# Performance work log

Hardware: AMD Instinct MI355X
Metric: run time of the kernel (lower is better)

The kernel has to match this reference:

```python
import jax, jax.numpy as jnp
import numpy as np

FS = 100
KERNEL = FS * 3 + 1  # 301, matches nn.AvgPool1d(kernel_size, stride=1, padding=K//2, count_include_pad=True)


def _avg_pool1d(x, k):
    # x: [B, L] -> same-length moving average with zero padding counted in the divisor
    w = jnp.full((1, 1, k), 1.0 / k, dtype=x.dtype)
    y = jax.lax.conv_general_dilated(
        x[:, None, :], w, window_strides=(1,), padding=[(k // 2, k // 2)],
        dimension_numbers=("NCH", "OIH", "NCH"))
    return y[:, 0, :]


def _unwrap_phase(phase):
    # torch-faithful np.unwrap: [B, L]
    d = jnp.diff(phase, axis=-1)
    dm = jnp.mod(d + jnp.pi, 2.0 * jnp.pi) - jnp.pi
    dm = jnp.where((dm == -jnp.pi) & (d > 0), jnp.pi, dm)
    offset = jnp.cumsum(d - dm, axis=-1)
    unwrapped = jnp.concatenate([phase[..., :1], phase[..., 1:] + offset], axis=-1)
    return jnp.nan_to_num(unwrapped, nan=0.0)


def _normalize(x):
    # zero mean, unit (unbiased, like torch.std) variance along last dim
    n = x.shape[-1]
    mean = jnp.mean(x, axis=-1, keepdims=True)
    var = jnp.sum((x - mean) ** 2, axis=-1, keepdims=True) / (n - 1)
    return (x - mean) / (jnp.sqrt(var) + 1e-5)


def setup_inputs() -> dict:
    key = jax.random.key(0)
    k1, k2 = jax.random.split(key)
    B, L = 64, 262144
    return {
        "radar_i": jax.random.normal(k1, (B, L), dtype=jnp.float32),
        "radar_q": jax.random.normal(k2, (B, L), dtype=jnp.float32),
    }


def reference(radar_i, radar_q):
    magnitude = jnp.nan_to_num(jnp.sqrt(radar_i ** 2 + radar_q ** 2), nan=0.0)
    phase = jnp.nan_to_num(jnp.arctan2(radar_q, radar_i), nan=0.0)
    phase_unwrap = _unwrap_phase(phase)
    phase_filt = phase_unwrap - _avg_pool1d(phase_unwrap, KERNEL)
    magnitude_filt = magnitude - _avg_pool1d(magnitude, KERNEL)
    magnitude_norm = jnp.nan_to_num(_normalize(magnitude_filt), nan=0.0)
    phase_norm = jnp.nan_to_num(_normalize(phase_filt), nan=0.0)
    return jnp.stack([magnitude_norm, phase_norm], axis=1)  # [B, 2, L]
```

## Files before the change

### kernel.cpp

```cpp
#include <hip/hip_runtime.h>
#include <math.h>
#include <stdint.h>

#define TPB 256
constexpr int Bn = 64;
constexpr int Ln = 262144;
constexpr int S  = 2048;
constexpr int NC = Ln / S;
constexpr int HA = S + 301;
constexpr int EPT = 11;
constexpr int OPT = S / TPB;
constexpr int NF4 = 641;
constexpr int LDSZ = 2820;
constexpr int NW = TPB / 64;

constexpr float TWO_PI_F = 6.28318530717958647692f;
constexpr float PI_F = 3.14159265358979323846f;
constexpr float HALF_PI_F = 1.57079632679489661923f;
constexpr float INV_TWO_PI_F = 0.15915494309189533577f;

__device__ __forceinline__ int wrap_k(float d) {
    float kf = floorf(__fmaf_rn(d, INV_TWO_PI_F, 0.5f));
    float dm = __fmaf_rn(-kf, TWO_PI_F, d);
    if (dm == -PI_F && d > 0.f) kf -= 1.f;
    return (int)kf;
}

__device__ __forceinline__ float fast_atan2f(float q, float i) {
    float aq = fabsf(q), ai = fabsf(i);
    float mx = fmaxf(aq, ai), mn = fminf(aq, ai);
    float r = __builtin_amdgcn_rcpf(mx);
    r = r * (2.0f - mx * r);
    float t = mn * r;
    if (mx == 0.f) t = 0.f;
    float s = t * t;
    float p = __fmaf_rn(s, 0.0028662257f, -0.0161657367f);
    p = __fmaf_rn(p, s,  0.0429096138f);
    p = __fmaf_rn(p, s, -0.0752896400f);
    p = __fmaf_rn(p, s,  0.1065626393f);
    p = __fmaf_rn(p, s, -0.1420889944f);
    p = __fmaf_rn(p, s,  0.1999355085f);
    p = __fmaf_rn(p, s, -0.3333314528f);
    float at = __fmaf_rn(p * s, t, t);
    if (aq > ai) at = HALF_PI_F - at;
    if (i < 0.f) at = PI_F - at;
    return (q < 0.f) ? -at : at;
}

__device__ __forceinline__ void gload_lds16(const float* g, float* lds_base) {
    __builtin_amdgcn_global_load_lds(
        (__attribute__((address_space(1))) void*)(uintptr_t)(const void*)g,
        (__attribute__((address_space(3))) void*)(uintptr_t)(void*)lds_base,
        16, 0, 0);
}

__global__ __launch_bounds__(TPB, 7) void k_filt(const float* __restrict__ Ig,
                                                 const float* __restrict__ Qg,
                                                 int* __restrict__ Ag,
                                                 int* __restrict__ Bg,
                                                 float* __restrict__ out,
                                                 float* __restrict__ PS) {
    __shared__ __align__(16) float sI_s[LDSZ];
    __shared__ __align__(16) float sQ_s[LDSZ];
    __shared__ int iwt[NW];
    __shared__ float fwt[NW];
    __shared__ float fwt2[NW];
    __shared__ float rbuf[NW][4];
    float* spu = sI_s + 1;
    float* smg = sQ_s + 1;

    const int c = blockIdx.x, b = blockIdx.y;
    const int t0 = c * S;
    const int base = t0 - 151;
    const int astart = base - 1;
    const int tid = threadIdx.x;
    const int lane = tid & 63, wid = tid >> 6;
    const bool edge = (c == 0) | (c == NC - 1);
    const float* Ib = Ig + (size_t)b * Ln;
    const float* Qb = Qg + (size_t)b * Ln;

    if (!edge) {
        const float* gI = Ib + astart;
        const float* gQ = Qb + astart;
#pragma unroll
        for (int k = wid; k < 11; k += NW) {
            int f = k * 64 + lane;
            if (f < NF4) {
                gload_lds16(gI + 4 * f, sI_s + k * 256);
                gload_lds16(gQ + 4 * f, sQ_s + k * 256);
            }
        }
    } else {
#pragma unroll
        for (int j = 0; j < 10; ++j) {
            int k = tid + j * TPB;
            int g = astart + k;
            float a = 0.f, q = 0.f;
            if (g >= 0 && g < Ln) { a = Ib[g]; q = Qb[g]; }
            sI_s[k] = a;
            sQ_s[k] = q;
        }
    }
    __syncthreads();

    const int seg = tid * EPT;
    const int kb = seg;
    const int gs = astart + kb;

    float ph[12], mg[12];
#pragma unroll
    for (int i = 0; i < 12; ++i) {
        float a = sI_s[kb + i], q = sQ_s[kb + i];
        ph[i] = fast_atan2f(q, a);
        mg[i] = __builtin_amdgcn_sqrtf(__fmaf_rn(a, a, q * q));
    }

    int kloc[12];
    kloc[0] = 0;
    float rm = 0.f;
    {
        int run = 0;
#pragma unroll
        for (int i = 1; i < 12; ++i) {
            run += wrap_k(ph[i] - ph[i - 1]);
            kloc[i] = run;
            rm += mg[i];
        }
    }

    int vi_ = kloc[11];
    float vf = rm;
#pragma unroll
    for (int o = 1; o < 64; o <<= 1) {
        int ui = __shfl_up(vi_, o, 64);
        float uf = __shfl_up(vf, o, 64);
        if (lane >= o) { vi_ += ui; vf += uf; }
    }
    if (lane == 63) { iwt[wid] = vi_; fwt[wid] = vf; }
    __syncthreads();
    int addi = 0; float addf = 0.f;
#pragma unroll
    for (int w = 0; w < NW; ++w) {
        addi += (w < wid) ? iwt[w] : 0;
        addf += (w < wid) ? fwt[w] : 0.f;
    }
    const int excl = vi_ - kloc[11] + addi;
    const float em = vf - rm + addf;

    if (tid == 13)  Ag[b * NC + c] = excl + kloc[8];
    if (tid == 199) Bg[b * NC + c] = excl + kloc[10];

    float rp = 0.f;
    if (!edge) {
#pragma unroll
        for (int i = 1; i < 12; ++i)
            rp += __fmaf_rn((float)(excl + kloc[i]), TWO_PI_F, ph[i]);
    } else {
#pragma unroll
        for (int i = 1; i < 12; ++i) {
            int g = gs + i;
            if (g >= 0 && g < Ln)
                rp += __fmaf_rn((float)(excl + kloc[i]), TWO_PI_F, ph[i]);
        }
    }

    float incf = rp;
#pragma unroll
    for (int o = 1; o < 64; o <<= 1) {
        float uf = __shfl_up(incf, o, 64);
        if (lane >= o) incf += uf;
    }
    if (lane == 63) fwt2[wid] = incf;
    __syncthreads();
    float addp = 0.f;
#pragma unroll
    for (int w = 0; w < NW; ++w) addp += (w < wid) ? fwt2[w] : 0.f;
    const float ep = incf - rp + addp;

    if (!edge) {
        float runp = ep, runm = em;
#pragma unroll
        for (int i = 1; i < 12; ++i) {
            int li = seg + i - 1;
            runp += __fmaf_rn((float)(excl + kloc[i]), TWO_PI_F, ph[i]);
            spu[li] = runp;
            runm += mg[i];
            smg[li] = runm;
        }
    } else {
        float runp = ep, runm = em;
#pragma unroll
        for (int i = 1; i < 12; ++i) {
            int li = seg + i - 1;
            int g = gs + i;
            float v = 0.f;
            if (g >= 0 && g < Ln)
                v = __fmaf_rn((float)(excl + kloc[i]), TWO_PI_F, ph[i]);
            runp += v;
            spu[li] = runp;
            runm += mg[i];
            smg[li] = runm;
        }
    }
    __syncthreads();

    float s1mf = 0.f, s2mf = 0.f, s1pf = 0.f, s2pf = 0.f;
    float* om = out + ((size_t)b * 2) * Ln + t0;
    float* op = out + ((size_t)b * 2 + 1) * Ln + t0;
    constexpr float INV_K = 1.0f / 301.0f;
#pragma unroll
    for (int j = 0; j < OPT; ++j) {
        int t = tid + j * TPB;
        int lt = t + 151;
        float Mq = smg[lt - 151], Mm = smg[lt - 1], Ml = smg[lt], Mp = smg[lt + 150];
        float Pq = spu[lt - 151], Pm = spu[lt - 1], Pl = spu[lt], Pp = spu[lt + 150];
        float fm = (Ml - Mm) - (Mp - Mq) * INV_K;
        float fp = (Pl - Pm) - (Pp - Pq) * INV_K;
        om[t] = fm;
        op[t] = fp;
        s1mf += fm; s2mf = __fmaf_rn(fm, fm, s2mf);
        s1pf += fp; s2pf = __fmaf_rn(fp, fp, s2pf);
    }
#pragma unroll
    for (int o = 32; o > 0; o >>= 1) {
        s1mf += __shfl_down(s1mf, o, 64);
        s2mf += __shfl_down(s2mf, o, 64);
        s1pf += __shfl_down(s1pf, o, 64);
        s2pf += __shfl_down(s2pf, o, 64);
    }
    if (lane == 0) { rbuf[wid][0] = s1mf; rbuf[wid][1] = s2mf; rbuf[wid][2] = s1pf; rbuf[wid][3] = s2pf; }
    __syncthreads();
    if (tid == 0) {
        float t0f = 0.f, t1f = 0.f, t2f = 0.f, t3f = 0.f;
#pragma unroll
        for (int w = 0; w < NW; ++w) {
            t0f += rbuf[w][0]; t1f += rbuf[w][1]; t2f += rbuf[w][2]; t3f += rbuf[w][3];
        }
        float* p = PS + (size_t)(b * NC + c) * 4;
        p[0] = t0f; p[1] = t1f; p[2] = t2f; p[3] = t3f;
    }
}

__global__ void k_post(const int* __restrict__ Ag, const int* __restrict__ Bg,
                       float* __restrict__ out, const float* __restrict__ PS,
                       float* __restrict__ ROW) {
    const int b = blockIdx.x;
    const int lane = threadIdx.x;
    const int idx = b * NC;

    int w = (Bg[idx + lane] - Ag[idx + lane]);
    if (lane + 64 < NC - 1) w += (Bg[idx + 64 + lane] - Ag[idx + 64 + lane]);
#pragma unroll
    for (int o = 32; o > 0; o >>= 1) w += __shfl_down(w, o, 64);
    int O = __shfl(w, 0, 64);
    int aL = Ag[idx + NC - 1];
    float C = TWO_PI_F * (float)(O - aL);

    constexpr float INV_K = 1.0f / 301.0f;
    float* op = out + ((size_t)b * 2 + 1) * Ln;
    double sd = 0.0, sd2 = 0.0;
#pragma unroll
    for (int k = 0; k < 3; ++k) {
        int j = lane + k * 64;
        if (j < 150) {
            int t = Ln - 150 + j;
            float delta = C * (float)(j + 1) * INV_K;
            float v = op[t];
            float nv = v + delta;
            op[t] = nv;
            sd += (double)delta;
            sd2 += (double)nv * (double)nv - (double)v * (double)v;
        }
    }

    const float* p1 = PS + (size_t)(idx + lane) * 4;
    const float* p2 = PS + (size_t)(idx + 64 + lane) * 4;
    double a0 = (double)p1[0] + (double)p2[0];
    double a1 = (double)p1[1] + (double)p2[1];
    double a2 = (double)p1[2] + (double)p2[2] + sd;
    double a3 = (double)p1[3] + (double)p2[3] + sd2;
#pragma unroll
    for (int o = 32; o > 0; o >>= 1) {
        a0 += __shfl_down(a0, o, 64);
        a1 += __shfl_down(a1, o, 64);
        a2 += __shfl_down(a2, o, 64);
        a3 += __shfl_down(a3, o, 64);
    }
    if (lane == 0) {
        double Ld = (double)Ln;
        double mm = a0 / Ld;
        double vm = (a1 - a0 * a0 / Ld) / (Ld - 1.0); vm = vm > 0 ? vm : 0;
        double mp = a2 / Ld;
        double vp = (a3 - a2 * a2 / Ld) / (Ld - 1.0); vp = vp > 0 ? vp : 0;
        float* r = ROW + b * 4;
        r[0] = (float)mm;
        r[1] = (float)(1.0 / (sqrt(vm) + 1e-5));
        r[2] = (float)mp;
        r[3] = (float)(1.0 / (sqrt(vp) + 1e-5));
    }
}

__global__ __launch_bounds__(256) void k_norm(float* __restrict__ out,
                                              const float* __restrict__ ROW) {
    const size_t n4 = (size_t)Bn * 2 * Ln / 4;
    size_t stride = (size_t)gridDim.x * blockDim.x;
    for (size_t p4 = (size_t)blockIdx.x * blockDim.x + threadIdx.x; p4 < n4; p4 += stride) {
        size_t p = p4 * 4;
        int b = (int)(p >> 19);
        int sig = (int)((p >> 18) & 1);
        float mean = ROW[b * 4 + sig * 2];
        float scale = ROW[b * 4 + sig * 2 + 1];
        float4 v = reinterpret_cast<float4*>(out)[p4];
        v.x = (v.x - mean) * scale;
        v.y = (v.y - mean) * scale;
        v.z = (v.z - mean) * scale;
        v.w = (v.w - mean) * scale;
        reinterpret_cast<float4*>(out)[p4] = v;
    }
}

extern "C" void kernel_launch(void* const* d_in, const int* in_sizes, int n_in,
                              void* d_out, int out_size, void* d_ws, size_t ws_size,
                              hipStream_t stream) {
    const float* Ig = (const float*)d_in[0];
    const float* Qg = (const float*)d_in[1];
    float* out = (float*)d_out;
    char* ws = (char*)d_ws;
    int* Ag = (int*)ws;
    int* Bg = (int*)(ws + 32768);
    float* PS = (float*)(ws + 65536);
    float* ROW = (float*)(ws + 65536 + (size_t)Bn * NC * 4 * sizeof(float));

    dim3 grid(NC, Bn);
    hipLaunchKernelGGL(k_filt, grid, dim3(TPB), 0, stream, Ig, Qg, Ag, Bg, out, PS);
    hipLaunchKernelGGL(k_post, dim3(Bn), dim3(64), 0, stream, Ag, Bg, out, PS, ROW);
    hipLaunchKernelGGL(k_norm, dim3(4096), dim3(256), 0, stream, out, ROW);
}
```

Measured before the change: 98.80 us.

## Use 12-element per-thread segments with float4 LDS reads/writes and vectorized outputs

```diff
diff --git a/kernel.cpp b/kernel.cpp
--- a/kernel.cpp
+++ b/kernel.cpp
@@ -8,10 +8,9 @@
 constexpr int S  = 2048;
 constexpr int NC = Ln / S;
 constexpr int HA = S + 301;
-constexpr int EPT = 11;
-constexpr int OPT = S / TPB;
+constexpr int EPT = 12;
 constexpr int NF4 = 641;
-constexpr int LDSZ = 2820;
+constexpr int LDSZ = 3076;
 constexpr int NW = TPB / 64;
 
 constexpr float TWO_PI_F = 6.28318530717958647692f;
@@ -54,7 +53,7 @@
         16, 0, 0);
 }
 
-__global__ __launch_bounds__(TPB, 7) void k_filt(const float* __restrict__ Ig,
+__global__ __launch_bounds__(TPB, 6) void k_filt(const float* __restrict__ Ig,
                                                  const float* __restrict__ Qg,
                                                  int* __restrict__ Ag,
                                                  int* __restrict__ Bg,
@@ -66,8 +65,6 @@
     __shared__ float fwt[NW];
     __shared__ float fwt2[NW];
     __shared__ float rbuf[NW][4];
-    float* spu = sI_s + 1;
-    float* smg = sQ_s + 1;
 
     const int c = blockIdx.x, b = blockIdx.y;
     const int t0 = c * S;
@@ -103,32 +100,47 @@
     }
     __syncthreads();
 
-    const int seg = tid * EPT;
-    const int kb = seg;
-    const int gs = astart + kb;
-
-    float ph[12], mg[12];
-#pragma unroll
-    for (int i = 0; i < 12; ++i) {
-        float a = sI_s[kb + i], q = sQ_s[kb + i];
-        ph[i] = fast_atan2f(q, a);
-        mg[i] = __builtin_amdgcn_sqrtf(__fmaf_rn(a, a, q * q));
-    }
-
-    int kloc[12];
+    const int s0 = EPT * tid;
+    const int gs = astart + s0;
+
+    float av[13], qv[13];
+    {
+        float4 a0 = *reinterpret_cast<const float4*>(sI_s + s0);
+        float4 a1 = *reinterpret_cast<const float4*>(sI_s + s0 + 4);
+        float4 a2 = *reinterpret_cast<const float4*>(sI_s + s0 + 8);
+        float  a3 = sI_s[s0 + 12];
+        float4 q0 = *reinterpret_cast<const float4*>(sQ_s + s0);
+        float4 q1 = *reinterpret_cast<const float4*>(sQ_s + s0 + 4);
+        float4 q2 = *reinterpret_cast<const float4*>(sQ_s + s0 + 8);
+        float  q3 = sQ_s[s0 + 12];
+        av[0]=a0.x; av[1]=a0.y; av[2]=a0.z; av[3]=a0.w;
+        av[4]=a1.x; av[5]=a1.y; av[6]=a1.z; av[7]=a1.w;
+        av[8]=a2.x; av[9]=a2.y; av[10]=a2.z; av[11]=a2.w; av[12]=a3;
+        qv[0]=q0.x; qv[1]=q0.y; qv[2]=q0.z; qv[3]=q0.w;
+        qv[4]=q1.x; qv[5]=q1.y; qv[6]=q1.z; qv[7]=q1.w;
+        qv[8]=q2.x; qv[9]=q2.y; qv[10]=q2.z; qv[11]=q2.w; qv[12]=q3;
+    }
+    float ph[13], mg[13];
+#pragma unroll
+    for (int i = 0; i < 13; ++i) {
+        ph[i] = fast_atan2f(qv[i], av[i]);
+        mg[i] = __builtin_amdgcn_sqrtf(__fmaf_rn(av[i], av[i], qv[i] * qv[i]));
+    }
+
+    int kloc[13];
     kloc[0] = 0;
     float rm = 0.f;
     {
         int run = 0;
 #pragma unroll
-        for (int i = 1; i < 12; ++i) {
+        for (int i = 1; i < 13; ++i) {
             run += wrap_k(ph[i] - ph[i - 1]);
             kloc[i] = run;
             rm += mg[i];
         }
     }
 
-    int vi_ = kloc[11];
+    int vi_ = kloc[12];
     float vf = rm;
 #pragma unroll
     for (int o = 1; o < 64; o <<= 1) {
@@ -144,20 +156,20 @@
         addi += (w < wid) ? iwt[w] : 0;
         addf += (w < wid) ? fwt[w] : 0.f;
     }
-    const int excl = vi_ - kloc[11] + addi;
+    const int excl = vi_ - kloc[12] + addi;
     const float em = vf - rm + addf;
 
-    if (tid == 13)  Ag[b * NC + c] = excl + kloc[8];
-    if (tid == 199) Bg[b * NC + c] = excl + kloc[10];
+    if (tid == 12)  Ag[b * NC + c] = excl + kloc[7];
+    if (tid == 183) Bg[b * NC + c] = excl + kloc[3];
 
     float rp = 0.f;
     if (!edge) {
 #pragma unroll
-        for (int i = 1; i < 12; ++i)
+        for (int i = 1; i < 13; ++i)
             rp += __fmaf_rn((float)(excl + kloc[i]), TWO_PI_F, ph[i]);
     } else {
 #pragma unroll
-        for (int i = 1; i < 12; ++i) {
+        for (int i = 1; i < 13; ++i) {
             int g = gs + i;
             if (g >= 0 && g < Ln)
                 rp += __fmaf_rn((float)(excl + kloc[i]), TWO_PI_F, ph[i]);
@@ -177,30 +189,36 @@
     for (int w = 0; w < NW; ++w) addp += (w < wid) ? fwt2[w] : 0.f;
     const float ep = incf - rp + addp;
 
-    if (!edge) {
+    {
+        float P[12], M[12];
         float runp = ep, runm = em;
-#pragma unroll
-        for (int i = 1; i < 12; ++i) {
-            int li = seg + i - 1;
-            runp += __fmaf_rn((float)(excl + kloc[i]), TWO_PI_F, ph[i]);
-            spu[li] = runp;
-            runm += mg[i];
-            smg[li] = runm;
-        }
-    } else {
-        float runp = ep, runm = em;
-#pragma unroll
-        for (int i = 1; i < 12; ++i) {
-            int li = seg + i - 1;
-            int g = gs + i;
-            float v = 0.f;
-            if (g >= 0 && g < Ln)
-                v = __fmaf_rn((float)(excl + kloc[i]), TWO_PI_F, ph[i]);
-            runp += v;
-            spu[li] = runp;
-            runm += mg[i];
-            smg[li] = runm;
-        }
+        if (!edge) {
+#pragma unroll
+            for (int i = 1; i < 13; ++i) {
+                runp += __fmaf_rn((float)(excl + kloc[i]), TWO_PI_F, ph[i]);
+                runm += mg[i];
+                P[i - 1] = runp;
+                M[i - 1] = runm;
+            }
+        } else {
+#pragma unroll
+            for (int i = 1; i < 13; ++i) {
+                int g = gs + i;
+                float v = 0.f;
+                if (g >= 0 && g < Ln)
+                    v = __fmaf_rn((float)(excl + kloc[i]), TWO_PI_F, ph[i]);
+                runp += v;
+                runm += mg[i];
+                P[i - 1] = runp;
+                M[i - 1] = runm;
+            }
+        }
+        *reinterpret_cast<float4*>(sI_s + s0)     = make_float4(P[0], P[1], P[2], P[3]);
+        *reinterpret_cast<float4*>(sI_s + s0 + 4) = make_float4(P[4], P[5], P[6], P[7]);
+        *reinterpret_cast<float4*>(sI_s + s0 + 8) = make_float4(P[8], P[9], P[10], P[11]);
+        *reinterpret_cast<float4*>(sQ_s + s0)     = make_float4(M[0], M[1], M[2], M[3]);
+        *reinterpret_cast<float4*>(sQ_s + s0 + 4) = make_float4(M[4], M[5], M[6], M[7]);
+        *reinterpret_cast<float4*>(sQ_s + s0 + 8) = make_float4(M[8], M[9], M[10], M[11]);
     }
     __syncthreads();
 
@@ -209,17 +227,38 @@
     float* op = out + ((size_t)b * 2 + 1) * Ln + t0;
     constexpr float INV_K = 1.0f / 301.0f;
 #pragma unroll
-    for (int j = 0; j < OPT; ++j) {
-        int t = tid + j * TPB;
-        int lt = t + 151;
-        float Mq = smg[lt - 151], Mm = smg[lt - 1], Ml = smg[lt], Mp = smg[lt + 150];
-        float Pq = spu[lt - 151], Pm = spu[lt - 1], Pl = spu[lt], Pp = spu[lt + 150];
-        float fm = (Ml - Mm) - (Mp - Mq) * INV_K;
-        float fp = (Pl - Pm) - (Pp - Pq) * INV_K;
-        om[t] = fm;
-        op[t] = fp;
-        s1mf += fm; s2mf = __fmaf_rn(fm, fm, s2mf);
-        s1pf += fp; s2pf = __fmaf_rn(fp, fp, s2pf);
+    for (int g2 = 0; g2 < 2; ++g2) {
+        const int t = 4 * tid + (g2 << 10);
+        float4 P0 = *reinterpret_cast<const float4*>(sI_s + t);
+        float2 Pa = *reinterpret_cast<const float2*>(sI_s + t + 150);
+        float4 Pb = *reinterpret_cast<const float4*>(sI_s + t + 152);
+        float4 Pc = *reinterpret_cast<const float4*>(sI_s + t + 300);
+        float  Pd = sI_s[t + 304];
+        float4 M0 = *reinterpret_cast<const float4*>(sQ_s + t);
+        float2 Ma = *reinterpret_cast<const float2*>(sQ_s + t + 150);
+        float4 Mb = *reinterpret_cast<const float4*>(sQ_s + t + 152);
+        float4 Mc = *reinterpret_cast<const float4*>(sQ_s + t + 300);
+        float  Md = sQ_s[t + 304];
+
+        float4 fmv, fpv;
+        fmv.x = (Ma.y - Ma.x) - (Mc.y - M0.x) * INV_K;
+        fmv.y = (Mb.x - Ma.y) - (Mc.z - M0.y) * INV_K;
+        fmv.z = (Mb.y - Mb.x) - (Mc.w - M0.z) * INV_K;
+        fmv.w = (Mb.z - Mb.y) - (Md   - M0.w) * INV_K;
+        fpv.x = (Pa.y - Pa.x) - (Pc.y - P0.x) * INV_K;
+        fpv.y = (Pb.x - Pa.y) - (Pc.z - P0.y) * INV_K;
+        fpv.z = (Pb.y - Pb.x) - (Pc.w - P0.z) * INV_K;
+        fpv.w = (Pb.z - Pb.y) - (Pd   - P0.w) * INV_K;
+
+        *reinterpret_cast<float4*>(om + t) = fmv;
+        *reinterpret_cast<float4*>(op + t) = fpv;
+
+        s1mf += fmv.x + fmv.y + fmv.z + fmv.w;
+        s2mf = __fmaf_rn(fmv.x, fmv.x, s2mf); s2mf = __fmaf_rn(fmv.y, fmv.y, s2mf);
+        s2mf = __fmaf_rn(fmv.z, fmv.z, s2mf); s2mf = __fmaf_rn(fmv.w, fmv.w, s2mf);
+        s1pf += fpv.x + fpv.y + fpv.z + fpv.w;
+        s2pf = __fmaf_rn(fpv.x, fpv.x, s2pf); s2pf = __fmaf_rn(fpv.y, fpv.y, s2pf);
+        s2pf = __fmaf_rn(fpv.z, fpv.z, s2pf); s2pf = __fmaf_rn(fpv.w, fpv.w, s2pf);
     }
 #pragma unroll
     for (int o = 32; o > 0; o >>= 1) {
```

New measurement: 110.0 us. 1.11x slower.
